# Kernel tuning notes

Measured on AMD Instinct MI355X. Metric: run time of the kernel, lower is better.

Reference implementation:

```python
import jax, jax.numpy as jnp
import numpy as np

N_NODES = 32
N_HEADS = 4
HEAD_DIM = 64
NEG_SLOPE = 0.2  # PyG GATConv default LeakyReLU slope


def setup_inputs() -> dict:
    key = jax.random.key(0)
    ks = jax.random.split(key, 8)
    roi_feats = jax.random.normal(ks[0], (N_NODES, 256, 96, 96), dtype=jnp.float32)
    edge_index = jax.random.randint(ks[1], (2, 512), 0, N_NODES, dtype=jnp.int32)
    W = jax.random.normal(ks[2], (256, N_HEADS * HEAD_DIM), dtype=jnp.float32) * 0.0625
    a_src = jax.random.normal(ks[3], (N_HEADS, HEAD_DIM), dtype=jnp.float32) * 0.125
    a_dst = jax.random.normal(ks[4], (N_HEADS, HEAD_DIM), dtype=jnp.float32) * 0.125
    gat_bias = jnp.zeros((N_HEADS * HEAD_DIM,), dtype=jnp.float32)
    cls_W = jax.random.normal(ks[5], (256, 32), dtype=jnp.float32) * 0.0625
    cls_b = jnp.zeros((32,), dtype=jnp.float32)
    return {"roi_feats": roi_feats, "edge_index": edge_index, "W": W,
            "a_src": a_src, "a_dst": a_dst, "gat_bias": gat_bias,
            "cls_W": cls_W, "cls_b": cls_b}


def _gat_conv(x, edge_index, W, a_src, a_dst, bias):
    # x: [N, C]; edge_index: [2, E] (src row 0, dst row 1)
    N = x.shape[0]
    # PyG GATConv adds self-loops by default
    loops = jnp.arange(N, dtype=edge_index.dtype)
    src = jnp.concatenate([edge_index[0], loops])
    dst = jnp.concatenate([edge_index[1], loops])
    h = (x @ W).reshape(N, N_HEADS, HEAD_DIM)          # [N, H, F]
    alpha_s = jnp.einsum('nhf,hf->nh', h, a_src)       # [N, H]
    alpha_d = jnp.einsum('nhf,hf->nh', h, a_dst)
    e = alpha_s[src] + alpha_d[dst]                    # [E', H]
    e = jnp.where(e >= 0, e, NEG_SLOPE * e)            # LeakyReLU
    # segment softmax over incoming edges of each dst node
    m = jax.ops.segment_max(e, dst, num_segments=N)    # [N, H]
    ex = jnp.exp(e - m[dst])
    denom = jax.ops.segment_sum(ex, dst, num_segments=N)
    alpha = ex / denom[dst]                            # [E', H]
    out = jax.ops.segment_sum(alpha[:, :, None] * h[src], dst, num_segments=N)
    return out.reshape(N, N_HEADS * HEAD_DIM) + bias


def reference(roi_feats, edge_index, W, a_src, a_dst, gat_bias, cls_W, cls_b):
    # [N, C, H, W] -> [N, C] spatial mean pool
    x = roi_feats.mean(axis=(2, 3))
    x = _gat_conv(x, edge_index, W, a_src, a_dst, gat_bias)
    logit = jax.nn.silu(x) @ cls_W + cls_b             # [N, num_au]
    return logit
```

## Files before the change

kernel.cpp:

```cpp
#include <hip/hip_runtime.h>
#include <math.h>

#define N_NODES  32
#define N_HEADS  4
#define CDIM     256
#define HWPIX    9216
#define ROWF4    2304
#define E_BASE   512
#define E_TOT    544
#define NEG_SLOPE 0.2f
#define XS       257

__global__ __launch_bounds__(256, 4) void pool_kernel(const float* __restrict__ roi,
                                                      float* __restrict__ x) {
    const int wave = threadIdx.x >> 6, lane = threadIdx.x & 63;
    const int row = blockIdx.x * 4 + wave;
    const float4* p = reinterpret_cast<const float4*>(roi) + (size_t)row * ROWF4 + lane;

    float4 A[12], B[12];
    float s = 0.f;

#pragma unroll
    for (int j = 0; j < 12; ++j) A[j] = p[j * 64];
#pragma unroll
    for (int j = 0; j < 12; ++j) B[j] = p[(12 + j) * 64];
#pragma unroll
    for (int j = 0; j < 12; ++j) s += (A[j].x + A[j].y) + (A[j].z + A[j].w);
#pragma unroll
    for (int j = 0; j < 12; ++j) A[j] = p[(24 + j) * 64];
#pragma unroll
    for (int j = 0; j < 12; ++j) s += (B[j].x + B[j].y) + (B[j].z + B[j].w);
#pragma unroll
    for (int j = 0; j < 12; ++j) s += (A[j].x + A[j].y) + (A[j].z + A[j].w);

#pragma unroll
    for (int off = 32; off; off >>= 1) s += __shfl_down(s, off);
    if (lane == 0) x[row] = s * (1.0f / (float)HWPIX);
}

__global__ __launch_bounds__(256) void h_kernel(const float* __restrict__ x,
                                                const float* __restrict__ W,
                                                float* __restrict__ H) {
    const int b = blockIdx.x;
    const int s = b >> 3, colbase = (b & 7) * 32;
    const int t = threadIdx.x;
    __shared__ float xrow[CDIM];
    __shared__ float part[8][32];

    xrow[t] = x[s * CDIM + t];
    __syncthreads();

    const int j = t & 31, q = t >> 5;
    const float* wp = W + (size_t)(q * 32) * CDIM + colbase + j;
    const float* xq = &xrow[q * 32];
    float acc = 0.f;
#pragma unroll
    for (int i = 0; i < 32; ++i)
        acc += xq[i] * wp[(size_t)i * CDIM];
    part[q][j] = acc;
    __syncthreads();

    if (t < 32) {
        float a = 0.f;
#pragma unroll
        for (int qq = 0; qq < 8; ++qq) a += part[qq][t];
        H[s * CDIM + colbase + t] = a;
    }
}

__global__ __launch_bounds__(256) void gat_kernel(const int* __restrict__ edge_index,
                                                  const float* __restrict__ H,
                                                  const float* __restrict__ a_src,
                                                  const float* __restrict__ a_dst,
                                                  const float* __restrict__ gat_bias,
                                                  const float* __restrict__ cls_W,
                                                  const float* __restrict__ cls_b,
                                                  float* __restrict__ out) {
    const int n = blockIdx.x;
    const int t = threadIdx.x;

    __shared__ float    hs[N_NODES * XS];
    __shared__ __align__(16) float asl[CDIM];
    __shared__ __align__(16) float adl[CDIM];
    __shared__ float    als[N_NODES * N_HEADS];
    __shared__ float    adn[N_HEADS];
    __shared__ unsigned msegu[N_HEADS];
    __shared__ float    M[N_NODES * N_HEADS];
    __shared__ float    sv[CDIM];
    __shared__ float    cred[8][32];

    float4 hv[8];
#pragma unroll
    for (int k = 0; k < 8; ++k) hv[k] = ((const float4*)H)[t + k * 256];
    const float asr = a_src[t], adr = a_dst[t];
    const float gb = gat_bias[t];
    const int es0 = edge_index[t],       ed0 = edge_index[E_BASE + t];
    const int es1 = edge_index[256 + t], ed1 = edge_index[E_BASE + 256 + t];
    float cb = 0.f;
    if (t < 32) cb = cls_b[t];
    float cw[32];
    {
        const int j = t & 31, g = t >> 5;
#pragma unroll
        for (int i = 0; i < 32; ++i) cw[i] = cls_W[(g * 32 + i) * 32 + j];
    }

#pragma unroll
    for (int k = 0; k < 8; ++k) {
        const int i = (t + k * 256) * 4, s = i >> 8, c = i & 255;
        hs[s * XS + c + 0] = hv[k].x;
        hs[s * XS + c + 1] = hv[k].y;
        hs[s * XS + c + 2] = hv[k].z;
        hs[s * XS + c + 3] = hv[k].w;
    }
    asl[t] = asr;
    adl[t] = adr;
    if (t < 128) M[t] = 0.f;
    if (t < 4)   msegu[t] = 0u;
    __syncthreads();

    if (t < 132) {
        if (t < 128) {
            const int s = t >> 2, hd = t & 3;
            const float* hrow = &hs[s * XS + hd * 64];
            const float* av   = &asl[hd * 64];
            float acc = 0.f;
#pragma unroll 16
            for (int f = 0; f < 64; ++f) acc += hrow[f] * av[f];
            als[t] = acc;
        } else {
            const int hd = t - 128;
            const float* hrow = &hs[n * XS + hd * 64];
            const float* av   = &adl[hd * 64];
            float acc = 0.f;
#pragma unroll 16
            for (int f = 0; f < 64; ++f) acc += hrow[f] * av[f];
            adn[hd] = acc;
        }
    }
    __syncthreads();

    {
        const bool sl = (t < 32) && (t == n);
#pragma unroll
        for (int hd = 0; hd < 4; ++hd) {
            float best = -INFINITY;
            if (ed0 == n) {
                float v = als[es0 * 4 + hd] + adn[hd];
                best = fmaxf(best, (v >= 0.f) ? v : NEG_SLOPE * v);
            }
            if (ed1 == n) {
                float v = als[es1 * 4 + hd] + adn[hd];
                best = fmaxf(best, (v >= 0.f) ? v : NEG_SLOPE * v);
            }
            if (sl) {
                float v = als[n * 4 + hd] + adn[hd];
                best = fmaxf(best, (v >= 0.f) ? v : NEG_SLOPE * v);
            }
            if (best > -INFINITY) {
                const int iv = __float_as_int(best);
                const unsigned key = (iv < 0) ? ~(unsigned)iv
                                              : ((unsigned)iv | 0x80000000u);
                atomicMax(&msegu[hd], key);
            }
        }
    }
    __syncthreads();

    float mx[4];
#pragma unroll
    for (int hd = 0; hd < 4; ++hd) {
        const unsigned key = msegu[hd];
        const int im = (key & 0x80000000u) ? (int)(key & 0x7fffffffu) : (int)~key;
        mx[hd] = __int_as_float(im);
    }

    {
        const bool sl = (t < 32) && (t == n);
#pragma unroll
        for (int hd = 0; hd < 4; ++hd) {
            if (ed0 == n) {
                float v = als[es0 * 4 + hd] + adn[hd];
                v = (v >= 0.f) ? v : NEG_SLOPE * v;
                atomicAdd(&M[es0 * 4 + hd], expf(v - mx[hd]));
            }
            if (ed1 == n) {
                float v = als[es1 * 4 + hd] + adn[hd];
                v = (v >= 0.f) ? v : NEG_SLOPE * v;
                atomicAdd(&M[es1 * 4 + hd], expf(v - mx[hd]));
            }
            if (sl) {
                float v = als[n * 4 + hd] + adn[hd];
                v = (v >= 0.f) ? v : NEG_SLOPE * v;
                atomicAdd(&M[n * 4 + hd], expf(v - mx[hd]));
            }
        }
    }
    __syncthreads();

    {
        const int hd = t >> 6;
        float acc = 0.f, msum = 0.f;
#pragma unroll
        for (int s = 0; s < N_NODES; ++s) {
            const float m = M[s * 4 + hd];
            msum += m;
            acc += m * hs[s * XS + t];
        }
        const float v = acc / msum + gb;
        sv[t] = v / (1.0f + expf(-v));
    }
    __syncthreads();

    {
        const int j = t & 31, g = t >> 5;
        float a = 0.f;
#pragma unroll
        for (int i = 0; i < 32; ++i) a += sv[g * 32 + i] * cw[i];
        cred[g][j] = a;
    }
    __syncthreads();
    if (t < 32) {
        float s2 = cb;
#pragma unroll
        for (int g = 0; g < 8; ++g) s2 += cred[g][t];
        out[n * 32 + t] = s2;
    }
}

extern "C" void kernel_launch(void* const* d_in, const int* in_sizes, int n_in,
                              void* d_out, int out_size, void* d_ws, size_t ws_size,
                              hipStream_t stream) {
    const float* roi   = (const float*)d_in[0];
    const int*   eidx  = (const int*)d_in[1];
    const float* W     = (const float*)d_in[2];
    const float* a_src = (const float*)d_in[3];
    const float* a_dst = (const float*)d_in[4];
    const float* gbias = (const float*)d_in[5];
    const float* clsW  = (const float*)d_in[6];
    const float* clsb  = (const float*)d_in[7];
    float* out = (float*)d_out;

    float* x = (float*)d_ws;
    float* H = x + 8192;

    pool_kernel<<<(N_NODES * CDIM) / 4, 256, 0, stream>>>(roi, x);
    h_kernel<<<256, 256, 0, stream>>>(x, W, H);
    gat_kernel<<<N_NODES, 256, 0, stream>>>(eidx, H, a_src, a_dst,
                                            gbias, clsW, clsb, out);
}
```

Before: 59.15 us.

## Fuse projection and GAT kernels with a global atomic counter barrier

Merges the h_kernel projection and gat_kernel into one launch. All 256 blocks compute their H slice, then increment a device-scope counter, and the first 32 blocks spin until every block has arrived before running the attention and classifier stages. Consumer blocks also prefetch their parameters before the barrier. This removes one kernel launch and the gap between launches, but it adds a memset, a spin-wait that relies on all 256 blocks being co-resident, and larger shared-memory use for every block.

```diff
diff --git a/kernel.cpp b/kernel.cpp
--- a/kernel.cpp
+++ b/kernel.cpp
@@ -10,6 +10,7 @@
 #define E_TOT    544
 #define NEG_SLOPE 0.2f
 #define XS       257
+#define HGRID    256
 
 __global__ __launch_bounds__(256, 4) void pool_kernel(const float* __restrict__ roi,
                                                       float* __restrict__ x) {
@@ -38,47 +39,22 @@
     if (lane == 0) x[row] = s * (1.0f / (float)HWPIX);
 }
 
-__global__ __launch_bounds__(256) void h_kernel(const float* __restrict__ x,
-                                                const float* __restrict__ W,
-                                                float* __restrict__ H) {
-    const int b = blockIdx.x;
-    const int s = b >> 3, colbase = (b & 7) * 32;
-    const int t = threadIdx.x;
+__global__ __launch_bounds__(256) void hgat_kernel(const float* __restrict__ x,
+                                                   const float* __restrict__ W,
+                                                   const int*   __restrict__ edge_index,
+                                                   const float* __restrict__ a_src,
+                                                   const float* __restrict__ a_dst,
+                                                   const float* __restrict__ gat_bias,
+                                                   const float* __restrict__ cls_W,
+                                                   const float* __restrict__ cls_b,
+                                                   float*       __restrict__ H,
+                                                   unsigned*    __restrict__ counter,
+                                                   float*       __restrict__ out) {
+    const int b = blockIdx.x, t = threadIdx.x;
+    const bool consumer = (b < N_NODES);
+
     __shared__ float xrow[CDIM];
     __shared__ float part[8][32];
-
-    xrow[t] = x[s * CDIM + t];
-    __syncthreads();
-
-    const int j = t & 31, q = t >> 5;
-    const float* wp = W + (size_t)(q * 32) * CDIM + colbase + j;
-    const float* xq = &xrow[q * 32];
-    float acc = 0.f;
-#pragma unroll
-    for (int i = 0; i < 32; ++i)
-        acc += xq[i] * wp[(size_t)i * CDIM];
-    part[q][j] = acc;
-    __syncthreads();
-
-    if (t < 32) {
-        float a = 0.f;
-#pragma unroll
-        for (int qq = 0; qq < 8; ++qq) a += part[qq][t];
-        H[s * CDIM + colbase + t] = a;
-    }
-}
-
-__global__ __launch_bounds__(256) void gat_kernel(const int* __restrict__ edge_index,
-                                                  const float* __restrict__ H,
-                                                  const float* __restrict__ a_src,
-                                                  const float* __restrict__ a_dst,
-                                                  const float* __restrict__ gat_bias,
-                                                  const float* __restrict__ cls_W,
-                                                  const float* __restrict__ cls_b,
-                                                  float* __restrict__ out) {
-    const int n = blockIdx.x;
-    const int t = threadIdx.x;
-
     __shared__ float    hs[N_NODES * XS];
     __shared__ __align__(16) float asl[CDIM];
     __shared__ __align__(16) float adl[CDIM];
@@ -89,21 +65,59 @@
     __shared__ float    sv[CDIM];
     __shared__ float    cred[8][32];
 
+    float asr = 0.f, adr = 0.f, gb = 0.f, cb = 0.f;
+    int es0 = 0, ed0 = -1, es1 = 0, ed1 = -1;
+    float cw[32];
+    if (consumer) {
+        asr = a_src[t]; adr = a_dst[t]; gb = gat_bias[t];
+        es0 = edge_index[t];       ed0 = edge_index[E_BASE + t];
+        es1 = edge_index[256 + t]; ed1 = edge_index[E_BASE + 256 + t];
+        if (t < 32) cb = cls_b[t];
+        const int j = t & 31, g = t >> 5;
+#pragma unroll
+        for (int i = 0; i < 32; ++i) cw[i] = cls_W[(g * 32 + i) * 32 + j];
+    }
+
+    {
+        const int s = b >> 3, colbase = (b & 7) * 32;
+        xrow[t] = x[s * CDIM + t];
+        __syncthreads();
+        const int j = t & 31, q = t >> 5;
+        const float* wp = W + (size_t)(q * 32) * CDIM + colbase + j;
+        const float* xq = &xrow[q * 32];
+        float acc = 0.f;
+#pragma unroll
+        for (int i = 0; i < 32; ++i)
+            acc += xq[i] * wp[(size_t)i * CDIM];
+        part[q][j] = acc;
+        __syncthreads();
+        if (t < 32) {
+            float a = 0.f;
+#pragma unroll
+            for (int qq = 0; qq < 8; ++qq) a += part[qq][t];
+            H[s * CDIM + colbase + t] = a;
+        }
+    }
+    __threadfence();
+    __syncthreads();
+    if (t == 0)
+        __hip_atomic_fetch_add(counter, 1u, __ATOMIC_RELEASE,
+                               __HIP_MEMORY_SCOPE_AGENT);
+    if (!consumer) return;
+
+    if (t == 0) {
+        while (__hip_atomic_load(counter, __ATOMIC_RELAXED,
+                                 __HIP_MEMORY_SCOPE_AGENT) < HGRID)
+            __builtin_amdgcn_s_sleep(2);
+        __threadfence();
+    }
+    __syncthreads();
+
+    const int n = b;
+
     float4 hv[8];
 #pragma unroll
     for (int k = 0; k < 8; ++k) hv[k] = ((const float4*)H)[t + k * 256];
-    const float asr = a_src[t], adr = a_dst[t];
-    const float gb = gat_bias[t];
-    const int es0 = edge_index[t],       ed0 = edge_index[E_BASE + t];
-    const int es1 = edge_index[256 + t], ed1 = edge_index[E_BASE + 256 + t];
-    float cb = 0.f;
-    if (t < 32) cb = cls_b[t];
-    float cw[32];
-    {
-        const int j = t & 31, g = t >> 5;
-#pragma unroll
-        for (int i = 0; i < 32; ++i) cw[i] = cls_W[(g * 32 + i) * 32 + j];
-    }
 
 #pragma unroll
     for (int k = 0; k < 8; ++k) {
@@ -241,11 +255,12 @@
     const float* clsb  = (const float*)d_in[7];
     float* out = (float*)d_out;
 
-    float* x = (float*)d_ws;
-    float* H = x + 8192;
-
+    unsigned* counter = (unsigned*)d_ws;
+    float*    x       = (float*)((char*)d_ws + 256);
+    float*    H       = x + 8192;
+
+    hipMemsetAsync(d_ws, 0, 64, stream);
     pool_kernel<<<(N_NODES * CDIM) / 4, 256, 0, stream>>>(roi, x);
-    h_kernel<<<256, 256, 0, stream>>>(x, W, H);
-    gat_kernel<<<N_NODES, 256, 0, stream>>>(eidx, H, a_src, a_dst,
-                                            gbias, clsW, clsb, out);
+    hgat_kernel<<<HGRID, 256, 0, stream>>>(x, W, eidx, a_src, a_dst,
+                                           gbias, clsW, clsb, H, counter, out);
 }
```

Result: slower. 81.98 us (+38.6%).
